# Kernel tuning notes

Measured on AMD Instinct MI355X. Metric: run time of the kernel, lower is better.

Reference implementation:

```python
import jax, jax.numpy as jnp
import numpy as np


def setup_inputs() -> dict:
    key = jax.random.key(0)
    k1, k2, k3 = jax.random.split(key, 3)
    B, C, H, W = 16, 256, 32, 32
    K, D = 8192, 256
    z = jax.random.normal(k1, (B, C, H, W), dtype=jnp.float32)
    # torch init: uniform(-1/K, 1/K); use small-scale values for realism
    embedding = jax.random.uniform(k2, (K, D), dtype=jnp.float32,
                                   minval=-1.0 / K, maxval=1.0 / K)
    proj_w = jax.random.normal(k3, (D, D), dtype=jnp.float32) * (1.0 / np.sqrt(D))
    return {"z": z, "embedding": embedding, "proj_w": proj_w}


def reference(z, embedding, proj_w):
    commitment_cost = 0.25
    B, C, H, W = z.shape
    # codebook = Linear(embedding) with no bias: emb @ W^T  -> [K, D]
    codebook = embedding @ proj_w.T
    zt = jnp.transpose(z, (0, 2, 3, 1))            # [B, H, W, C]
    zf = zt.reshape(-1, C)                          # [N, C], N = B*H*W
    # squared distances: ||z||^2 + ||e||^2 - 2 z.e  -> [N, K]
    d = (jnp.sum(zf * zf, axis=1, keepdims=True)
         + jnp.sum(codebook * codebook, axis=1)
         - 2.0 * jnp.einsum('nd,kd->nk', zf, codebook))
    min_encoding_indices = jnp.argmin(d, axis=1)    # [N]
    z_quantized = codebook[min_encoding_indices].reshape(zt.shape)  # [B,H,W,C]
    commitment_loss = commitment_cost * jnp.mean(
        (jax.lax.stop_gradient(z_quantized) - zt) ** 2)
    codebook_loss = jnp.mean((z_quantized - jax.lax.stop_gradient(zt)) ** 2)
    loss = commitment_loss + codebook_loss
    # straight-through estimator
    zq_st = zt + jax.lax.stop_gradient(z_quantized - zt)
    out = jnp.transpose(zq_st, (0, 3, 1, 2))        # [B, C, H, W]
    idx = min_encoding_indices.reshape(B, H, W)
    return out, loss, commitment_loss, codebook_loss, idx
```

## Files before the change

### kernel.cpp

```cpp
#include <hip/hip_runtime.h>
#include <cfloat>


constexpr int Dd = 256;
constexpr float INV_M = 1.0f / 4194304.0f;
constexpr float DLT = 8e-4f;
constexpr int SLOTS = 128;

typedef unsigned short u16;
typedef unsigned int u32;
typedef __attribute__((ext_vector_type(8))) short short8;
typedef __attribute__((ext_vector_type(4))) float f32x4;

__device__ __forceinline__ unsigned monof(float f) {
  unsigned u = __float_as_uint(f);
  return (u & 0x80000000u) ? ~u : (u | 0x80000000u);
}
__device__ __forceinline__ float unmonof(unsigned p) {
  unsigned u = (p & 0x80000000u) ? (p & 0x7FFFFFFFu) : ~p;
  return __uint_as_float(u);
}
__device__ __forceinline__ u16 f2bf(float x) {
  unsigned u = __float_as_uint(x);
  u += 0x7FFFu + ((u >> 16) & 1u);
  return (u16)(u >> 16);
}

__global__ __launch_bounds__(256)
void k_codebook(const float* __restrict__ emb, const float* __restrict__ proj,
                float* __restrict__ cb, u16* __restrict__ ef) {
  __shared__ __align__(16) float et[64 * 68];
  __shared__ __align__(16) float pt[64 * 68];
  __shared__ __align__(16) u16 tileT[64 * 72];
  const int t = threadIdx.x;
  const int tx = t & 15, ty = t >> 4;
  const int kb = blockIdx.x * 64;
  const int db = blockIdx.y * 64;
  float acc[4][4];
#pragma unroll
  for (int u = 0; u < 4; ++u)
#pragma unroll
    for (int v = 0; v < 4; ++v) acc[u][v] = 0.f;

  const int jm = t & 15;
  const int q  = t >> 4;

  for (int jc = 0; jc < Dd; jc += 64) {
    __syncthreads();
#pragma unroll
    for (int i = 0; i < 4; ++i) {
      const int row = q + i * 16;
      const float4 e4 = *(const float4*)(emb  + (size_t)(kb + row) * Dd + jc + jm * 4);
      const float4 p4 = *(const float4*)(proj + (size_t)(db + row) * Dd + jc + jm * 4);
      et[(jm*4 + 0) * 68 + row] = e4.x;
      et[(jm*4 + 1) * 68 + row] = e4.y;
      et[(jm*4 + 2) * 68 + row] = e4.z;
      et[(jm*4 + 3) * 68 + row] = e4.w;
      pt[(jm*4 + 0) * 68 + row] = p4.x;
      pt[(jm*4 + 1) * 68 + row] = p4.y;
      pt[(jm*4 + 2) * 68 + row] = p4.z;
      pt[(jm*4 + 3) * 68 + row] = p4.w;
    }
    __syncthreads();
#pragma unroll 16
    for (int j = 0; j < 64; ++j) {
      const float4 a4 = *(const float4*)(et + j * 68 + ty * 4);
      const float4 b4 = *(const float4*)(pt + j * 68 + tx * 4);
      const float a[4] = {a4.x, a4.y, a4.z, a4.w};
      const float b[4] = {b4.x, b4.y, b4.z, b4.w};
#pragma unroll
      for (int u = 0; u < 4; ++u)
#pragma unroll
        for (int v = 0; v < 4; ++v) acc[u][v] = fmaf(a[u], b[v], acc[u][v]);
    }
  }
#pragma unroll
  for (int u = 0; u < 4; ++u) {
    const int k = kb + ty*4 + u;
#pragma unroll
    for (int v = 0; v < 4; ++v) {
      const int d = db + tx*4 + v;
      const float val = acc[u][v];
      cb[(size_t)k * Dd + d] = val;
      tileT[(ty*4 + u) * 72 + tx*4 + v] = f2bf(val);
    }
  }
  __syncthreads();
  uint4* ef16 = (uint4*)ef;
#pragma unroll
  for (int w2 = 0; w2 < 2; ++w2) {
    const int uu = w2 * 256 + t;
    const int k16g = uu >> 7;
    const int d32g = (uu >> 6) & 1;
    const int ln   = uu & 63;
    const int klo  = k16g * 16 + (ln & 15);
    const int dlo  = d32g * 32 + (ln >> 4) * 8;
    ef16[((kb >> 4) + k16g) * 512 + ((db >> 5) + d32g) * 64 + ln] =
        *(const uint4*)&tileT[klo * 72 + dlo];
  }
}

__global__ __launch_bounds__(256)
void k_norms(const float* __restrict__ cb, float* __restrict__ norms) {
  const int k = blockIdx.x * 256 + threadIdx.x;
  const float* row = cb + (size_t)k * Dd;
  float s = 0.f;
  for (int d = 0; d < Dd; d += 4) {
    const float4 v = *(const float4*)(row + d);
    s = fmaf(v.x, v.x, s);
    s = fmaf(v.y, v.y, s);
    s = fmaf(v.z, v.z, s);
    s = fmaf(v.w, v.w, s);
  }
  norms[k] = s;
}

__global__ __launch_bounds__(256)
void k_prep_z(const float* __restrict__ z, u16* __restrict__ zf,
              float* __restrict__ znorm) {
  __shared__ float tile[256 * 33];
  const int t = threadIdx.x;
  const int blk = blockIdx.x;
  const int w = t & 31, rg = t >> 5;
  const size_t zbase = (size_t)(blk >> 5) * 262144 + (size_t)(blk & 31) * 32 + w;
#pragma unroll 8
  for (int i = 0; i < 32; ++i) {
    const int d = rg * 32 + i;
    tile[d * 33 + w] = z[zbase + (size_t)d * 1024];
  }
  __syncthreads();
  if (t < 32) {
    float s = 0.f;
    for (int d = 0; d < Dd; ++d) {
      const float v = tile[d * 33 + t];
      s = fmaf(v, v, s);
    }
    znorm[blk * 32 + t] = s;
  }
  const int ml16 = t & 15;
  const int seg  = (t >> 4) & 7;
  const int hi   = t >> 7;
  const int nl   = hi * 16 + ml16;
  uint4* zf16 = (uint4*)zf;
  const int ubase = ((blk * 2 + hi) * 8 + seg) * 64 + ml16;
#pragma unroll
  for (int j = 0; j < 4; ++j) {
    u16 hb[8];
#pragma unroll
    for (int e = 0; e < 8; ++e)
      hb[e] = f2bf(tile[(seg * 32 + j * 8 + e) * 33 + nl]);
    zf16[ubase + j * 16] = *(const uint4*)hb;
  }
}

__global__ __launch_bounds__(256, 2)
void k_scan(const u16* __restrict__ zf, const u16* __restrict__ ef,
            const float* __restrict__ norms, const float* __restrict__ znorm,
            u32* __restrict__ rowminG, u32* __restrict__ rowcnt,
            u32* __restrict__ slots) {
  const int t    = threadIdx.x;
  const int lane = t & 63;
  const int ml   = lane & 15;
  const int qd   = lane >> 4;
  const int wvu  = __builtin_amdgcn_readfirstlane(t >> 6);
  const int rowhalf = wvu & 1;
  const int colhalf = wvu >> 1;
  const int bid  = blockIdx.x;
  const int kb   = (bid & 7) * 1024;
  const int nb   = (bid >> 3) * 64;

  const uint4* zf16 = (const uint4*)zf;
  const uint4* ef16 = (const uint4*)ef;
  const uint4* eb = ef16 + (size_t)((kb >> 4) + colhalf * 8) * 512 + lane;

  short8 A[2][8];
  {
    const uint4* za = zf16 + (size_t)((nb >> 4) + rowhalf * 2) * 512 + lane;
#pragma unroll
    for (int rt = 0; rt < 2; ++rt)
#pragma unroll
      for (int d32 = 0; d32 < 8; ++d32)
        A[rt][d32] = *(const short8*)(za + rt * 512 + d32 * 64);
  }

  float zn[2][4];
#pragma unroll
  for (int rt = 0; rt < 2; ++rt) {
    const int nr = nb + rowhalf * 32 + rt * 16 + qd * 4;
    const f32x4 z4 = *(const f32x4*)(znorm + nr);
#pragma unroll
    for (int r = 0; r < 4; ++r) zn[rt][r] = z4[r];
  }

  short8 Bq[4][4];
#pragma unroll
  for (int s = 0; s < 4; ++s)
#pragma unroll
    for (int ct = 0; ct < 4; ++ct)
      Bq[s][ct] = *(const short8*)(eb + ct * 512 + s * 64);

#pragma unroll 1
  for (int kt = 0; kt < 4; ++kt) {
    const size_t ekt = (size_t)kt * 16 * 512;
#pragma unroll
    for (int cq = 0; cq < 2; ++cq) {
      const uint4* ecq = eb + ekt + (size_t)(cq * 4) * 512;

      f32x4 acc[2][4];
#pragma unroll
      for (int rt = 0; rt < 2; ++rt)
#pragma unroll
        for (int ct = 0; ct < 4; ++ct) acc[rt][ct] = (f32x4)0.f;

#pragma unroll
      for (int d32 = 0; d32 < 8; ++d32) {
        const int st = d32 & 3;
#pragma unroll
        for (int ct = 0; ct < 4; ++ct)
#pragma unroll
          for (int rt = 0; rt < 2; ++rt)
            acc[rt][ct] = __builtin_amdgcn_mfma_f32_16x16x32_bf16(
                A[rt][d32], Bq[st][ct], acc[rt][ct], 0, 0, 0);
        const bool last4 = (kt == 3) && (cq == 1) && (d32 >= 4);
        if (!last4) {
          const uint4* pn;
          if (d32 < 4) {
            pn = ecq + (d32 + 4) * 64;
          } else if (cq == 0) {
            pn = eb + ekt + (size_t)4 * 512 + (d32 - 4) * 64;
          } else {
            pn = eb + ekt + (size_t)16 * 512 + (d32 - 4) * 64;
          }
#pragma unroll
          for (int ct = 0; ct < 4; ++ct)
            Bq[st][ct] = *(const short8*)(pn + ct * 512);
        }
      }

#pragma unroll
      for (int ct = 0; ct < 4; ++ct) {
        const int k0 = kb + kt * 256 + colhalf * 128 + cq * 64 + ct * 16 + ml;
        const float nkv = norms[k0];
#pragma unroll
        for (int rt = 0; rt < 2; ++rt)
#pragma unroll
          for (int r = 0; r < 4; ++r)
            acc[rt][ct][r] = (zn[rt][r] + nkv) - 2.0f * acc[rt][ct][r];
      }

      float m2[2][4];
#pragma unroll
      for (int rt = 0; rt < 2; ++rt)
#pragma unroll
        for (int r = 0; r < 4; ++r) {
          float m = fminf(fminf(acc[rt][0][r], acc[rt][1][r]),
                          fminf(acc[rt][2][r], acc[rt][3][r]));
#pragma unroll
          for (int s = 1; s < 16; s <<= 1) m = fminf(m, __shfl_xor(m, s, 64));
          m2[rt][r] = m;
        }

      unsigned myg = 0xFFFFFFFFu;
      if (ml < 8) {
        const int rt_ = ml >> 2, r_ = ml & 3;
        const int n = nb + rowhalf * 32 + rt_ * 16 + qd * 4 + r_;
        const unsigned pk = monof(m2[rt_][r_]);
        const unsigned old = atomicMin(&rowminG[n], pk);
        myg = min(old, pk);
      }
      float thrv[2][4];
#pragma unroll
      for (int rt = 0; rt < 2; ++rt)
#pragma unroll
        for (int r = 0; r < 4; ++r) {
          const unsigned gg = __shfl(myg, (lane & 48) + rt * 4 + r, 64);
          thrv[rt][r] = unmonof(gg) + DLT;
        }

#pragma unroll
      for (int ct = 0; ct < 4; ++ct) {
        const int k = kb + kt * 256 + colhalf * 128 + cq * 64 + ct * 16 + ml;
#pragma unroll
        for (int rt = 0; rt < 2; ++rt)
#pragma unroll
          for (int r = 0; r < 4; ++r) {
            if (acc[rt][ct][r] <= thrv[rt][r]) {
              const int n = nb + rowhalf * 32 + rt * 16 + qd * 4 + r;
              const u32 pos = atomicAdd(&rowcnt[n], 1u);
              if (pos < (u32)SLOTS) {
                const float e = acc[rt][ct][r] - zn[rt][r];
                int q = __float2int_rn(e * 2097152.0f) + 262144;
                q = q < 0 ? 0 : (q > 524287 ? 524287 : q);
                slots[n * SLOTS + pos] = ((u32)q << 13) | (u32)k;
              }
            }
          }
      }
    }
  }
}

__global__ __launch_bounds__(256)
void k_rescore(const float* __restrict__ z, const float* __restrict__ cb,
               const float* __restrict__ norms, const float* __restrict__ znorm,
               const u32* __restrict__ rowminG, const u32* __restrict__ rowcnt,
               const u32* __restrict__ slots,
               unsigned long long* __restrict__ packed) {
  __shared__ float ztl[32 * 261];
  const int t = threadIdx.x;
  const int blk = blockIdx.x;
  const int w = t & 31, dg = t >> 5;
  const size_t zbase = (size_t)(blk >> 5) * 262144 + (size_t)(blk & 31) * 32;
#pragma unroll 8
  for (int i = 0; i < 32; ++i) {
    const int d = dg * 32 + i;
    ztl[w * 261 + d] = z[zbase + (size_t)d * 1024 + w];
  }
  __syncthreads();

  const int lane = t & 63;
  const int wv = t >> 6;
#pragma unroll 1
  for (int i = 0; i < 8; ++i) {
    const int rl = wv * 8 + i;
    const int n = blk * 32 + rl;
    const u32 cnt = rowcnt[n];
    const float znr = znorm[n];
    const float* zp = ztl + rl * 261 + lane * 4;
    const float g = unmonof(rowminG[n]);
    const int qThr = __float2int_rn((g + DLT - znr) * 2097152.0f) + 262144 + 68;
    unsigned long long best = 0xFFFFFFFFFFFFFFFFull;
    if (cnt <= (u32)SLOTS) {
      for (u32 c = 0; c < cnt; ++c) {
        const u32 v = slots[n * SLOTS + c];
        if ((int)(v >> 13) > qThr) continue;
        const int k = (int)(v & 8191u);
        const float4 c4 = *(const float4*)(cb + (size_t)k * Dd + lane * 4);
        float p = 0.f;
        p = fmaf(zp[0], c4.x, p);
        p = fmaf(zp[1], c4.y, p);
        p = fmaf(zp[2], c4.z, p);
        p = fmaf(zp[3], c4.w, p);
#pragma unroll
        for (int s = 1; s < 64; s <<= 1) p += __shfl_xor(p, s, 64);
        const float sc = (znr + norms[k]) - 2.0f * p;
        const unsigned long long pk =
            ((unsigned long long)monof(sc) << 32) | (unsigned)k;
        if (pk < best) best = pk;
      }
    } else {
      for (int k = 0; k < 8192; ++k) {
        const float4 c4 = *(const float4*)(cb + (size_t)k * Dd + lane * 4);
        float p = 0.f;
        p = fmaf(zp[0], c4.x, p);
        p = fmaf(zp[1], c4.y, p);
        p = fmaf(zp[2], c4.z, p);
        p = fmaf(zp[3], c4.w, p);
#pragma unroll
        for (int s = 1; s < 64; s <<= 1) p += __shfl_xor(p, s, 64);
        const float sc = (znr + norms[k]) - 2.0f * p;
        const unsigned long long pk =
            ((unsigned long long)monof(sc) << 32) | (unsigned)k;
        if (pk < best) best = pk;
      }
    }
    if (lane == 0 && cnt > 0) packed[n] = best;
  }
}

__global__ __launch_bounds__(256)
void k_output(const float* __restrict__ z, const float* __restrict__ cb,
              const unsigned long long* __restrict__ packed,
              float* __restrict__ out, float* __restrict__ idxf,
              float* __restrict__ ssum) {
  __shared__ float zqT[256 * 33];
  __shared__ float part[4];
  const int t = threadIdx.x;
  const int blk = blockIdx.x;
  const int nbase = blk * 32;

  {
    const int nl = t >> 3, m = t & 7;
    const int idx = (int)(packed[nbase + nl] & 0xFFFFFFFFull) & 8191;
    const float* row = cb + (size_t)idx * Dd;
#pragma unroll
    for (int i = 0; i < 8; ++i) {
      const int d0 = m * 4 + i * 32;
      const float4 v = *(const float4*)(row + d0);
      zqT[(d0 + 0) * 33 + nl] = v.x;
      zqT[(d0 + 1) * 33 + nl] = v.y;
      zqT[(d0 + 2) * 33 + nl] = v.z;
      zqT[(d0 + 3) * 33 + nl] = v.w;
    }
    if (t < 32)
      idxf[nbase + t] = (float)(unsigned)(packed[nbase + t] & 0xFFFFFFFFull);
  }
  __syncthreads();

  const int w = t & 31, cg = t >> 5;
  const size_t base = (size_t)(blk >> 5) * 262144 + (size_t)(blk & 31) * 32 + w;
  float local = 0.f;
#pragma unroll
  for (int cc = 0; cc < 32; ++cc) {
    const int c = cg * 32 + cc;
    const float q  = zqT[c * 33 + w];
    const float zv = z[base + (size_t)c * 1024];
    out[base + (size_t)c * 1024] = q;
    const float dd = q - zv;
    local = fmaf(dd, dd, local);
  }
  float v = local;
#pragma unroll
  for (int m = 1; m < 64; m <<= 1) v += __shfl_xor(v, m, 64);
  if ((t & 63) == 0) part[t >> 6] = v;
  __syncthreads();
  if (t == 0) atomicAdd(ssum, part[0] + part[1] + part[2] + part[3]);
}

__global__ void k_final(const float* __restrict__ ssum, float* __restrict__ scal) {
  const float m = *ssum * INV_M;
  scal[0] = 1.25f * m;
  scal[1] = 0.25f * m;
  scal[2] = m;
}

extern "C" void kernel_launch(void* const* d_in, const int* in_sizes, int n_in,
                              void* d_out, int out_size, void* d_ws, size_t ws_size,
                              hipStream_t stream) {
  const float* z    = (const float*)d_in[0];
  const float* emb  = (const float*)d_in[1];
  const float* proj = (const float*)d_in[2];

  float* out  = (float*)d_out;
  float* scal = out + 4194304;
  float* idxf = out + 4194307;

  float* cb    = (float*)d_ws;
  float* norms = cb + 2097152;
  unsigned long long* packed =
      (unsigned long long*)(norms + 8192);
  float* znorm = (float*)(packed + 16384);
  u16* zf = (u16*)(znorm + 16384);
  u16* ef = zf + 4194304;
  u32* rowminG = (u32*)(ef + 2097152);
  u32* rowcnt = rowminG + 16384;
  u32* slots = rowcnt + 16384;
  float* ssum = (float*)(slots + (size_t)16384 * SLOTS);

  hipMemsetAsync(rowminG, 0xFF, 16384 * sizeof(u32), stream);
  hipMemsetAsync(rowcnt, 0, 16384 * sizeof(u32), stream);
  hipMemsetAsync(packed, 0xFF, 16384 * sizeof(unsigned long long), stream);
  hipMemsetAsync(ssum, 0, sizeof(float), stream);

  k_codebook<<<dim3(128, 4), 256, 0, stream>>>(emb, proj, cb, ef);
  k_norms   <<<32, 256, 0, stream>>>(cb, norms);
  k_prep_z  <<<512, 256, 0, stream>>>(z, zf, znorm);
  k_scan    <<<2048, 256, 0, stream>>>(zf, ef, norms, znorm,
                                       rowminG, rowcnt, slots);
  k_rescore <<<512, 256, 0, stream>>>(z, cb, norms, znorm,
                                      rowminG, rowcnt, slots, packed);
  k_output  <<<512, 256, 0, stream>>>(z, cb, packed, out, idxf, ssum);
  k_final   <<<1, 1, 0, stream>>>(ssum, scal);

  (void)in_sizes; (void)n_in; (void)out_size; (void)ws_size;
}
```

Measured before the change: 374.2 us.

## Stage z tile in LDS and shrink register prefetch to raise scan occupancy

The z operand tile for each scan block is now copied into shared memory with global_load_lds and read per d32 step, replacing the 64 short8 A registers held per thread. The B prefetch queue is cut from four stages to two double-buffered stages. The launch bound moves from 2 to 4 blocks per SIMD. Together these lower register pressure so more waves can hide the latency of the global codebook loads, at the cost of extra LDS reads per MFMA group and a shallower prefetch distance for B.

New measurement: 361.9 us. 1.03x faster.

```diff
diff --git a/kernel.cpp b/kernel.cpp
--- a/kernel.cpp
+++ b/kernel.cpp
@@ -11,6 +11,9 @@
 typedef unsigned int u32;
 typedef __attribute__((ext_vector_type(8))) short short8;
 typedef __attribute__((ext_vector_type(4))) float f32x4;
+
+#define GLOBAL_AS __attribute__((address_space(1)))
+#define LDS_AS    __attribute__((address_space(3)))
 
 __device__ __forceinline__ unsigned monof(float f) {
   unsigned u = __float_as_uint(f);
@@ -153,11 +156,12 @@
   }
 }
 
-__global__ __launch_bounds__(256, 2)
+__global__ __launch_bounds__(256, 4)
 void k_scan(const u16* __restrict__ zf, const u16* __restrict__ ef,
             const float* __restrict__ norms, const float* __restrict__ znorm,
             u32* __restrict__ rowminG, u32* __restrict__ rowcnt,
             u32* __restrict__ slots) {
+  __shared__ __align__(16) u16 zsh[64 * 256];
   const int t    = threadIdx.x;
   const int lane = t & 63;
   const int ml   = lane & 15;
@@ -171,17 +175,22 @@
 
   const uint4* zf16 = (const uint4*)zf;
   const uint4* ef16 = (const uint4*)ef;
+
+  {
+    const uint4* zsrc = zf16 + (size_t)(nb >> 4) * 512;
+#pragma unroll
+    for (int i = 0; i < 8; ++i) {
+      const int g = wvu * 512 + i * 64;
+      __builtin_amdgcn_global_load_lds((const GLOBAL_AS void*)(zsrc + g + lane),
+                                       (LDS_AS void*)(zsh + (size_t)g * 8), 16, 0, 0);
+    }
+  }
+  __syncthreads();
+
+  const u16* ab0 = zsh + (size_t)((rowhalf * 2 + 0) * 8) * 512 + lane * 8;
+  const u16* ab1 = zsh + (size_t)((rowhalf * 2 + 1) * 8) * 512 + lane * 8;
+
   const uint4* eb = ef16 + (size_t)((kb >> 4) + colhalf * 8) * 512 + lane;
-
-  short8 A[2][8];
-  {
-    const uint4* za = zf16 + (size_t)((nb >> 4) + rowhalf * 2) * 512 + lane;
-#pragma unroll
-    for (int rt = 0; rt < 2; ++rt)
-#pragma unroll
-      for (int d32 = 0; d32 < 8; ++d32)
-        A[rt][d32] = *(const short8*)(za + rt * 512 + d32 * 64);
-  }
 
   float zn[2][4];
 #pragma unroll
@@ -192,12 +201,14 @@
     for (int r = 0; r < 4; ++r) zn[rt][r] = z4[r];
   }
 
-  short8 Bq[4][4];
-#pragma unroll
-  for (int s = 0; s < 4; ++s)
-#pragma unroll
-    for (int ct = 0; ct < 4; ++ct)
-      Bq[s][ct] = *(const short8*)(eb + ct * 512 + s * 64);
+  short8 As0[2], As1[2], Bb0[4], Bb1[4];
+  As0[0] = *(const short8*)(ab0);
+  As0[1] = *(const short8*)(ab1);
+#pragma unroll
+  for (int ct = 0; ct < 4; ++ct) {
+    Bb0[ct] = *(const short8*)(eb + ct * 512);
+    Bb1[ct] = *(const short8*)(eb + ct * 512 + 64);
+  }
 
 #pragma unroll 1
   for (int kt = 0; kt < 4; ++kt) {
@@ -214,26 +225,48 @@
 
 #pragma unroll
       for (int d32 = 0; d32 < 8; ++d32) {
-        const int st = d32 & 3;
-#pragma unroll
-        for (int ct = 0; ct < 4; ++ct)
-#pragma unroll
-          for (int rt = 0; rt < 2; ++rt)
-            acc[rt][ct] = __builtin_amdgcn_mfma_f32_16x16x32_bf16(
-                A[rt][d32], Bq[st][ct], acc[rt][ct], 0, 0, 0);
-        const bool last4 = (kt == 3) && (cq == 1) && (d32 >= 4);
-        if (!last4) {
+        const int dn = (d32 + 1) & 7;
+        if (d32 & 1) {
+          As0[0] = *(const short8*)(ab0 + dn * 512);
+          As0[1] = *(const short8*)(ab1 + dn * 512);
+        } else {
+          As1[0] = *(const short8*)(ab0 + dn * 512);
+          As1[1] = *(const short8*)(ab1 + dn * 512);
+        }
+        if (d32 & 1) {
+#pragma unroll
+          for (int ct = 0; ct < 4; ++ct)
+#pragma unroll
+            for (int rt = 0; rt < 2; ++rt)
+              acc[rt][ct] = __builtin_amdgcn_mfma_f32_16x16x32_bf16(
+                  As1[rt], Bb1[ct], acc[rt][ct], 0, 0, 0);
+        } else {
+#pragma unroll
+          for (int ct = 0; ct < 4; ++ct)
+#pragma unroll
+            for (int rt = 0; rt < 2; ++rt)
+              acc[rt][ct] = __builtin_amdgcn_mfma_f32_16x16x32_bf16(
+                  As0[rt], Bb0[ct], acc[rt][ct], 0, 0, 0);
+        }
+        const bool lastB = (kt == 3) && (cq == 1) && (d32 >= 6);
+        if (!lastB) {
           const uint4* pn;
-          if (d32 < 4) {
-            pn = ecq + (d32 + 4) * 64;
+          if (d32 < 6) {
+            pn = ecq + (d32 + 2) * 64;
           } else if (cq == 0) {
-            pn = eb + ekt + (size_t)4 * 512 + (d32 - 4) * 64;
+            pn = eb + ekt + (size_t)4 * 512 + (d32 - 6) * 64;
           } else {
-            pn = eb + ekt + (size_t)16 * 512 + (d32 - 4) * 64;
+            pn = eb + ekt + (size_t)16 * 512 + (d32 - 6) * 64;
           }
-#pragma unroll
-          for (int ct = 0; ct < 4; ++ct)
-            Bq[st][ct] = *(const short8*)(pn + ct * 512);
+          if (d32 & 1) {
+#pragma unroll
+            for (int ct = 0; ct < 4; ++ct)
+              Bb1[ct] = *(const short8*)(pn + ct * 512);
+          } else {
+#pragma unroll
+            for (int ct = 0; ct < 4; ++ct)
+              Bb0[ct] = *(const short8*)(pn + ct * 512);
+          }
         }
       }
 
```
